# Kernel optimization log

Hardware: AMD Instinct MI355X
Metric: run time of the kernel (lower is better)

The kernel has to match this reference:

```python
import jax, jax.numpy as jnp
import numpy as np

N = 12288   # num_nodes
D = 128     # isize
K_TOP = 31  # k + 1, per top_k(similarities, self.k + 1)


def setup_inputs() -> dict:
    key = jax.random.key(0)
    features = jax.random.normal(key, (N, D), dtype=jnp.float32)
    eye = jnp.eye(D, dtype=jnp.float32)  # param_init: weight <- I, bias <- 0
    return {
        "features": features,
        "W1": eye,
        "b1": jnp.zeros((D,), jnp.float32),
        "W2": eye,
        "b2": jnp.zeros((D,), jnp.float32),
    }


def reference(features, W1, b1, W2, b2):
    # internal_forward: Linear -> ReLU -> Linear (nlayers=2, act='relu')
    h = jax.nn.relu(features @ W1.T + b1)
    h = h @ W2.T + b2
    # F.normalize(h, dim=1, p=2) with eps=1e-12
    hn = h / jnp.maximum(jnp.linalg.norm(h, axis=1, keepdims=True), 1e-12)
    # dense N x N cosine similarity
    sim = hn @ hn.T
    # top_k: keep top (k+1) entries per row, zero elsewhere; then apply_non_linearity='relu'
    vals, idx = jax.lax.top_k(sim, K_TOP)          # [N, K_TOP]
    rows = jnp.arange(sim.shape[0])[:, None]       # [N, 1]
    # relu(sim * mask) == scatter relu(top-k values) into a zero matrix
    out = jnp.zeros_like(sim).at[rows, idx].set(jax.nn.relu(vals))
    return out
```

## Files before the change

kernel.cpp:

```cpp
#include <hip/hip_runtime.h>
#include <stdint.h>
#include <math.h>

#define NN 12288
#define DD 128
#define KTOP 31
#define TCAND 64
#define CCAP 128
#define RPB 16
#define WPB 8
#define LDEP 14
#define NSTREAM 32
#define KPR (NSTREAM * LDEP)
#define KPL (KPR / 64)
#define ITERS 48

typedef __attribute__((ext_vector_type(8))) short bf16x8;
typedef __attribute__((ext_vector_type(4))) float f32x4;

__device__ __forceinline__ unsigned short f2bf(float x) {
  unsigned int u = __float_as_uint(x);
  u += 0x7fffu + ((u >> 16) & 1u);
  return (unsigned short)(u >> 16);
}

__device__ __forceinline__ unsigned umed3(unsigned a, unsigned b, unsigned c) {
  unsigned d;
  asm("v_med3_u32 %0, %1, %2, %3" : "=v"(d) : "v"(a), "v"(b), "v"(c));
  return d;
}

#define PINS(P) { \
  const unsigned p_ = (P); \
  _Pragma("unroll") \
  for (int i_ = 0; i_ < LDEP - 1; ++i_) \
    L[i_] = umed3(p_, L[i_], L[i_ + 1]); \
  L[LDEP - 1] = L[LDEP - 1] > p_ ? L[LDEP - 1] : p_; }

__global__ __launch_bounds__(128)
void wtrans_kernel(const float* __restrict__ W1, const float* __restrict__ W2,
                   float* __restrict__ W1T, float* __restrict__ W2T) {
  const int r = blockIdx.x, c = threadIdx.x;
  W1T[(size_t)c * DD + r] = W1[(size_t)r * DD + c];
  W2T[(size_t)c * DD + r] = W2[(size_t)r * DD + c];
}

__global__ __launch_bounds__(256)
void mlp_norm_kernel(const float* __restrict__ feat,
                     const float* __restrict__ W1T, const float* __restrict__ b1,
                     const float* __restrict__ W2T, const float* __restrict__ b2,
                     double* __restrict__ hn64, unsigned short* __restrict__ hnb) {
  __shared__ double bufA[16][DD];
  __shared__ double bufB[16][DD];
  __shared__ double mnorm[16];
  const int t = threadIdx.x;
  const int c = t & 127;
  const int g = t >> 7;
  const int row0 = blockIdx.x * 16 + g * 8;

  #pragma unroll
  for (int rr = 0; rr < 8; ++rr)
    bufA[g * 8 + rr][c] = (double)feat[(size_t)(row0 + rr) * DD + c];
  __syncthreads();

  {
    double acc[8] = {0,0,0,0,0,0,0,0};
    for (int k = 0; k < DD; k += 2) {
      double w0 = (double)W1T[(size_t)k * DD + c];
      double w1 = (double)W1T[(size_t)(k + 1) * DD + c];
      #pragma unroll
      for (int rr = 0; rr < 8; ++rr) {
        double2 a2 = *(const double2*)(&bufA[g * 8 + rr][k]);
        acc[rr] = fma(w0, a2.x, acc[rr]);
        acc[rr] = fma(w1, a2.y, acc[rr]);
      }
    }
    double bb = (double)b1[c];
    #pragma unroll
    for (int rr = 0; rr < 8; ++rr)
      bufB[g * 8 + rr][c] = fmax(acc[rr] + bb, 0.0);
  }
  __syncthreads();
  {
    double acc[8] = {0,0,0,0,0,0,0,0};
    for (int k = 0; k < DD; k += 2) {
      double w0 = (double)W2T[(size_t)k * DD + c];
      double w1 = (double)W2T[(size_t)(k + 1) * DD + c];
      #pragma unroll
      for (int rr = 0; rr < 8; ++rr) {
        double2 a2 = *(const double2*)(&bufB[g * 8 + rr][k]);
        acc[rr] = fma(w0, a2.x, acc[rr]);
        acc[rr] = fma(w1, a2.y, acc[rr]);
      }
    }
    double bb = (double)b2[c];
    #pragma unroll
    for (int rr = 0; rr < 8; ++rr)
      bufA[g * 8 + rr][c] = acc[rr] + bb;
  }
  __syncthreads();

  const int lane = t & 63;
  const int w = t >> 6;
  #pragma unroll
  for (int r2 = 0; r2 < 4; ++r2) {
    int rr = w * 4 + r2;
    double x0 = bufA[rr][lane];
    double x1 = bufA[rr][lane + 64];
    double s = x0 * x0 + x1 * x1;
    #pragma unroll
    for (int d = 1; d < 64; d <<= 1)
      s += __shfl_xor(s, d);
    if (lane == 0) mnorm[rr] = fmax(sqrt(s), 1e-12);
  }
  __syncthreads();
  #pragma unroll
  for (int rr = 0; rr < 8; ++rr) {
    double v = bufA[g * 8 + rr][c] / mnorm[g * 8 + rr];
    hn64[(size_t)(row0 + rr) * DD + c] = v;
    hnb[(size_t)(row0 + rr) * DD + c] = f2bf((float)v);
  }
}

__global__ __launch_bounds__(512, 6)
void simsel_kernel(const unsigned short* __restrict__ hnb,
                   const double* __restrict__ hn64,
                   float* __restrict__ resval, int* __restrict__ rescol) {
  __shared__ unsigned keybuf[RPB][KPR + 1];
  __shared__ unsigned scand[WPB][CCAP];
  __shared__ double cres[WPB][CCAP];
  const int t = threadIdx.x, lane = t & 63, wv = t >> 6;
  const int m = lane & 15, quad = lane >> 4;
  const int row0 = blockIdx.x * RPB;

  bf16x8 afrag[4];
  #pragma unroll
  for (int kc = 0; kc < 4; ++kc)
    afrag[kc] = *(const bf16x8*)(hnb + (size_t)(row0 + m) * DD + kc * 32 + quad * 8);

  unsigned L[LDEP];
  #pragma unroll
  for (int i = 0; i < LDEP; ++i) L[i] = 0;

  for (int it = 0; it < ITERS; ++it) {
    const int cb = it * (WPB * 32) + wv * 32;
    f32x4 acc0 = {0.0f, 0.0f, 0.0f, 0.0f};
    f32x4 acc1 = {0.0f, 0.0f, 0.0f, 0.0f};
    #pragma unroll
    for (int kc = 0; kc < 4; ++kc) {
      bf16x8 b0 = *(const bf16x8*)(hnb + (size_t)(cb + m) * DD + kc * 32 + quad * 8);
      bf16x8 b1 = *(const bf16x8*)(hnb + (size_t)(cb + 16 + m) * DD + kc * 32 + quad * 8);
      acc0 = __builtin_amdgcn_mfma_f32_16x16x32_bf16(b0, afrag[kc], acc0, 0, 0, 0);
      acc1 = __builtin_amdgcn_mfma_f32_16x16x32_bf16(b1, afrag[kc], acc1, 0, 0, 0);
    }
    #pragma unroll
    for (int r = 0; r < 4; ++r) {
      {
        unsigned bf = f2bf(acc0[r]);
        unsigned s = (bf & 0x8000u) ? 0u : bf;
        unsigned p = (s << 16) | (unsigned)(cb + quad * 4 + r);
        PINS(p)
      }
      {
        unsigned bf = f2bf(acc1[r]);
        unsigned s = (bf & 0x8000u) ? 0u : bf;
        unsigned p = (s << 16) | (unsigned)(cb + 16 + quad * 4 + r);
        PINS(p)
      }
    }
  }

  #pragma unroll
  for (int d = 0; d < LDEP; ++d)
    keybuf[m][(wv * 4 + quad) * LDEP + d] = L[d];
  __syncthreads();

  for (int ii = 0; ii < 2; ++ii) {
    const int lr = wv * 2 + ii;
    const int grow = row0 + lr;
    unsigned k7[KPL];
    #pragma unroll
    for (int i = 0; i < KPL; ++i)
      k7[i] = keybuf[lr][lane * KPL + i];

    unsigned lo = 0, hi = 0xFFFFu;
    while (lo < hi) {
      unsigned mid = (lo + hi + 1) >> 1;
      int c = 0;
      #pragma unroll
      for (int i = 0; i < KPL; ++i) c += (int)((k7[i] >> 16) >= mid);
      #pragma unroll
      for (int d = 1; d < 64; d <<= 1) c += __shfl_xor(c, d);
      if (c >= TCAND) lo = mid; else hi = mid - 1;
    }
    const unsigned thr = lo;

    int cl = 0;
    #pragma unroll
    for (int i = 0; i < KPL; ++i) cl += (int)((k7[i] >> 16) >= thr);
    int pre = cl;
    #pragma unroll
    for (int d = 1; d < 64; d <<= 1) {
      int y = __shfl_up(pre, d);
      if (lane >= d) pre += y;
    }
    const int total = __shfl(pre, 63);
    const int nc = total < CCAP ? total : CCAP;
    int slot = pre - cl;
    #pragma unroll
    for (int i = 0; i < KPL; ++i) {
      if ((k7[i] >> 16) >= thr) {
        if (slot < CCAP) scand[wv][slot] = k7[i];
        ++slot;
      }
    }

    const double* arow = hn64 + (size_t)grow * DD;
    const int hl = lane >> 5;
    const int kl = (lane & 31) * 4;
    const double a0 = arow[kl], a1 = arow[kl + 1], a2 = arow[kl + 2], a3 = arow[kl + 3];
    const int ng = (nc + 1) >> 1;
    for (int g = 0; g < ng; ++g) {
      const int ci = 2 * g + hl;
      double partial = 0.0;
      if (ci < nc) {
        const int col = (int)(scand[wv][ci] & 0xFFFFu);
        const double* brow = hn64 + (size_t)col * DD + kl;
        double2 b01 = *(const double2*)(brow);
        double2 b23 = *(const double2*)(brow + 2);
        partial = fma(a0, b01.x, fma(a1, b01.y, fma(a2, b23.x, a3 * b23.y)));
      }
      #pragma unroll
      for (int d = 1; d < 32; d <<= 1)
        partial += __shfl_xor(partial, d);
      if ((lane & 31) == 0 && ci < nc) cres[wv][ci] = partial;
    }
    double rv0 = -1.0e300, rv1 = -1.0e300;
    int rc0 = 0x7fffffff, rc1 = 0x7fffffff;
    if (lane < nc)      { rv0 = cres[wv][lane];      rc0 = (int)(scand[wv][lane] & 0xFFFFu); }
    if (lane + 64 < nc) { rv1 = cres[wv][lane + 64]; rc1 = (int)(scand[wv][lane + 64] & 0xFFFFu); }

    for (int itk = 0; itk < KTOP; ++itk) {
      bool f = (rv0 > rv1) || (rv0 == rv1 && rc0 < rc1);
      double bv = f ? rv0 : rv1;
      int bc = f ? rc0 : rc1;
      #pragma unroll
      for (int d = 1; d < 64; d <<= 1) {
        double ov = __shfl_xor(bv, d);
        int    oc = __shfl_xor(bc, d);
        bool tk = (ov > bv) || (ov == bv && oc < bc);
        bv = tk ? ov : bv;
        bc = tk ? oc : bc;
      }
      if (lane == itk) {
        resval[(size_t)grow * KTOP + itk] = (float)fmax(bv, 0.0);
        rescol[(size_t)grow * KTOP + itk] = bc;
      }
      if (rv0 == bv && rc0 == bc) rv0 = -1.0e300;
      else if (rv1 == bv && rc1 == bc) rv1 = -1.0e300;
    }
  }
}

__global__ __launch_bounds__(256)
void emit_kernel(const float* __restrict__ resval, const int* __restrict__ rescol,
                 float* __restrict__ out) {
  const int row = blockIdx.x, t = threadIdx.x;
  float v = 0.0f; int c = 0;
  if (t < KTOP) {
    v = resval[(size_t)row * KTOP + t];
    c = rescol[(size_t)row * KTOP + t];
  }
  f32x4* orow = (f32x4*)(out + (size_t)row * NN);
  const f32x4 z = {0.0f, 0.0f, 0.0f, 0.0f};
  #pragma unroll
  for (int i = 0; i < NN / 4 / 256; ++i)
    __builtin_nontemporal_store(z, &orow[i * 256 + t]);
  __syncthreads();
  if (t < KTOP) out[(size_t)row * NN + c] = v;
}

extern "C" void kernel_launch(void* const* d_in, const int* in_sizes, int n_in,
                              void* d_out, int out_size, void* d_ws, size_t ws_size,
                              hipStream_t stream) {
  const float* feat = (const float*)d_in[0];
  const float* W1 = (const float*)d_in[1];
  const float* b1 = (const float*)d_in[2];
  const float* W2 = (const float*)d_in[3];
  const float* b2 = (const float*)d_in[4];
  float* out = (float*)d_out;

  double* hn64 = (double*)d_ws;
  unsigned short* hnb = (unsigned short*)(hn64 + (size_t)NN * DD);
  float* resval = (float*)(hnb + (size_t)NN * DD);
  int* rescol = (int*)(resval + (size_t)NN * KTOP);
  float* W1T = (float*)(rescol + (size_t)NN * KTOP);
  float* W2T = W1T + DD * DD;

  wtrans_kernel<<<DD, DD, 0, stream>>>(W1, W2, W1T, W2T);
  mlp_norm_kernel<<<NN / 16, 256, 0, stream>>>(feat, W1T, b1, W2T, b2, hn64, hnb);
  simsel_kernel<<<NN / RPB, 512, 0, stream>>>(hnb, hn64, resval, rescol);
  emit_kernel<<<NN, 256, 0, stream>>>(resval, rescol, out);
}
```

Before: 1.066 ms.

## Stage candidate tiles in LDS via async global_load_lds double buffering

```diff
diff --git a/kernel.cpp b/kernel.cpp
--- a/kernel.cpp
+++ b/kernel.cpp
@@ -13,7 +13,8 @@
 #define NSTREAM 32
 #define KPR (NSTREAM * LDEP)
 #define KPL (KPR / 64)
-#define ITERS 48
+#define SC 128
+#define NST (NN / SC)
 
 typedef __attribute__((ext_vector_type(8))) short bf16x8;
 typedef __attribute__((ext_vector_type(4))) float f32x4;
@@ -122,10 +123,11 @@
   }
 }
 
-__global__ __launch_bounds__(512, 6)
+__global__ __launch_bounds__(512, 2)
 void simsel_kernel(const unsigned short* __restrict__ hnb,
                    const double* __restrict__ hn64,
                    float* __restrict__ resval, int* __restrict__ rescol) {
+  __shared__ __attribute__((aligned(16))) unsigned short stage[2][SC * DD];
   __shared__ unsigned keybuf[RPB][KPR + 1];
   __shared__ unsigned scand[WPB][CCAP];
   __shared__ double cres[WPB][CCAP];
@@ -138,36 +140,59 @@
   for (int kc = 0; kc < 4; ++kc)
     afrag[kc] = *(const bf16x8*)(hnb + (size_t)(row0 + m) * DD + kc * 32 + quad * 8);
 
+  const unsigned short* gsrc[4];
+  unsigned ldsb[4];
+  #pragma unroll
+  for (int i = 0; i < 4; ++i) {
+    int u = i * 512 + t;
+    int col = u >> 4;
+    int ch = (u & 15) ^ (col & 7);
+    gsrc[i] = hnb + (size_t)col * DD + ch * 8;
+    ldsb[i] = (unsigned)(i * 8192 + wv * 1024);
+  }
+
+  unsigned roff[4];
+  #pragma unroll
+  for (int kc = 0; kc < 4; ++kc)
+    roff[kc] = (unsigned)((wv * 16 + m) * 256 + (((kc * 4 + quad) ^ (m & 7)) * 16));
+
   unsigned L[LDEP];
   #pragma unroll
   for (int i = 0; i < LDEP; ++i) L[i] = 0;
 
-  for (int it = 0; it < ITERS; ++it) {
-    const int cb = it * (WPB * 32) + wv * 32;
-    f32x4 acc0 = {0.0f, 0.0f, 0.0f, 0.0f};
-    f32x4 acc1 = {0.0f, 0.0f, 0.0f, 0.0f};
+  {
+    char* dst = (char*)stage[0];
+    #pragma unroll
+    for (int i = 0; i < 4; ++i)
+      __builtin_amdgcn_global_load_lds((const void*)gsrc[i], (void*)(dst + ldsb[i]), 16, 0, 0);
+  }
+  __syncthreads();
+
+  for (int s = 0; s < NST; ++s) {
+    if (s + 1 < NST) {
+      char* dst = (char*)stage[(s + 1) & 1];
+      const size_t gadd = (size_t)(s + 1) * (SC * DD);
+      #pragma unroll
+      for (int i = 0; i < 4; ++i)
+        __builtin_amdgcn_global_load_lds((const void*)(gsrc[i] + gadd),
+                                         (void*)(dst + ldsb[i]), 16, 0, 0);
+    }
+    const char* buf = (const char*)stage[s & 1];
+    f32x4 acc = {0.0f, 0.0f, 0.0f, 0.0f};
     #pragma unroll
     for (int kc = 0; kc < 4; ++kc) {
-      bf16x8 b0 = *(const bf16x8*)(hnb + (size_t)(cb + m) * DD + kc * 32 + quad * 8);
-      bf16x8 b1 = *(const bf16x8*)(hnb + (size_t)(cb + 16 + m) * DD + kc * 32 + quad * 8);
-      acc0 = __builtin_amdgcn_mfma_f32_16x16x32_bf16(b0, afrag[kc], acc0, 0, 0, 0);
-      acc1 = __builtin_amdgcn_mfma_f32_16x16x32_bf16(b1, afrag[kc], acc1, 0, 0, 0);
-    }
+      bf16x8 b = *(const bf16x8*)(buf + roff[kc]);
+      acc = __builtin_amdgcn_mfma_f32_16x16x32_bf16(b, afrag[kc], acc, 0, 0, 0);
+    }
+    const int cbw = s * SC + wv * 16;
     #pragma unroll
     for (int r = 0; r < 4; ++r) {
-      {
-        unsigned bf = f2bf(acc0[r]);
-        unsigned s = (bf & 0x8000u) ? 0u : bf;
-        unsigned p = (s << 16) | (unsigned)(cb + quad * 4 + r);
-        PINS(p)
-      }
-      {
-        unsigned bf = f2bf(acc1[r]);
-        unsigned s = (bf & 0x8000u) ? 0u : bf;
-        unsigned p = (s << 16) | (unsigned)(cb + 16 + quad * 4 + r);
-        PINS(p)
-      }
-    }
+      unsigned bf = f2bf(acc[r]);
+      unsigned sc = (bf & 0x8000u) ? 0u : bf;
+      unsigned p = (sc << 16) | (unsigned)(cbw + quad * 4 + r);
+      PINS(p)
+    }
+    __syncthreads();
   }
 
   #pragma unroll
```

Result: slower. 1.179 ms (+10.6%).

## Split similarity ladder and candidate selection into separate kernels

Applied to the files above, without the earlier changes.

```diff
diff --git a/kernel.cpp b/kernel.cpp
--- a/kernel.cpp
+++ b/kernel.cpp
@@ -9,10 +9,7 @@
 #define CCAP 128
 #define RPB 16
 #define WPB 8
-#define LDEP 14
-#define NSTREAM 32
-#define KPR (NSTREAM * LDEP)
-#define KPL (KPR / 64)
+#define LDEP 8
 #define ITERS 48
 
 typedef __attribute__((ext_vector_type(8))) short bf16x8;
@@ -30,12 +27,12 @@
   return d;
 }
 
-#define PINS(P) { \
+#define PINS8(Lx, P) { \
   const unsigned p_ = (P); \
   _Pragma("unroll") \
-  for (int i_ = 0; i_ < LDEP - 1; ++i_) \
-    L[i_] = umed3(p_, L[i_], L[i_ + 1]); \
-  L[LDEP - 1] = L[LDEP - 1] > p_ ? L[LDEP - 1] : p_; }
+  for (int i_ = 0; i_ < 7; ++i_) \
+    Lx[i_] = umed3(p_, Lx[i_], Lx[i_ + 1]); \
+  Lx[7] = Lx[7] > p_ ? Lx[7] : p_; }
 
 __global__ __launch_bounds__(128)
 void wtrans_kernel(const float* __restrict__ W1, const float* __restrict__ W2,
@@ -123,12 +120,8 @@
 }
 
 __global__ __launch_bounds__(512, 6)
-void simsel_kernel(const unsigned short* __restrict__ hnb,
-                   const double* __restrict__ hn64,
-                   float* __restrict__ resval, int* __restrict__ rescol) {
-  __shared__ unsigned keybuf[RPB][KPR + 1];
-  __shared__ unsigned scand[WPB][CCAP];
-  __shared__ double cres[WPB][CCAP];
+void simladder_kernel(const unsigned short* __restrict__ hnb,
+                      unsigned* __restrict__ kbuf) {
   const int t = threadIdx.x, lane = t & 63, wv = t >> 6;
   const int m = lane & 15, quad = lane >> 4;
   const int row0 = blockIdx.x * RPB;
@@ -138,9 +131,8 @@
   for (int kc = 0; kc < 4; ++kc)
     afrag[kc] = *(const bf16x8*)(hnb + (size_t)(row0 + m) * DD + kc * 32 + quad * 8);
 
-  unsigned L[LDEP];
-  #pragma unroll
-  for (int i = 0; i < LDEP; ++i) L[i] = 0;
+  unsigned LA[8] = {0,0,0,0,0,0,0,0};
+  unsigned LB[8] = {0,0,0,0,0,0,0,0};
 
   for (int it = 0; it < ITERS; ++it) {
     const int cb = it * (WPB * 32) + wv * 32;
@@ -159,106 +151,117 @@
         unsigned bf = f2bf(acc0[r]);
         unsigned s = (bf & 0x8000u) ? 0u : bf;
         unsigned p = (s << 16) | (unsigned)(cb + quad * 4 + r);
-        PINS(p)
+        PINS8(LA, p)
       }
       {
         unsigned bf = f2bf(acc1[r]);
         unsigned s = (bf & 0x8000u) ? 0u : bf;
         unsigned p = (s << 16) | (unsigned)(cb + 16 + quad * 4 + r);
-        PINS(p)
+        PINS8(LB, p)
       }
     }
   }
 
-  #pragma unroll
-  for (int d = 0; d < LDEP; ++d)
-    keybuf[m][(wv * 4 + quad) * LDEP + d] = L[d];
-  __syncthreads();
-
-  for (int ii = 0; ii < 2; ++ii) {
-    const int lr = wv * 2 + ii;
-    const int grow = row0 + lr;
-    unsigned k7[KPL];
-    #pragma unroll
-    for (int i = 0; i < KPL; ++i)
-      k7[i] = keybuf[lr][lane * KPL + i];
-
-    unsigned lo = 0, hi = 0xFFFFu;
-    while (lo < hi) {
-      unsigned mid = (lo + hi + 1) >> 1;
-      int c = 0;
-      #pragma unroll
-      for (int i = 0; i < KPL; ++i) c += (int)((k7[i] >> 16) >= mid);
-      #pragma unroll
-      for (int d = 1; d < 64; d <<= 1) c += __shfl_xor(c, d);
-      if (c >= TCAND) lo = mid; else hi = mid - 1;
-    }
-    const unsigned thr = lo;
-
-    int cl = 0;
-    #pragma unroll
-    for (int i = 0; i < KPL; ++i) cl += (int)((k7[i] >> 16) >= thr);
-    int pre = cl;
+  unsigned* dst = kbuf + (size_t)(row0 + m) * 512 + (wv * 4 + quad) * 16;
+  *(uint4*)(dst)      = make_uint4(LA[0], LA[1], LA[2], LA[3]);
+  *(uint4*)(dst + 4)  = make_uint4(LA[4], LA[5], LA[6], LA[7]);
+  *(uint4*)(dst + 8)  = make_uint4(LB[0], LB[1], LB[2], LB[3]);
+  *(uint4*)(dst + 12) = make_uint4(LB[4], LB[5], LB[6], LB[7]);
+}
+
+__global__ __launch_bounds__(256)
+void select_kernel(const unsigned* __restrict__ kbuf,
+                   const double* __restrict__ hn64,
+                   float* __restrict__ resval, int* __restrict__ rescol) {
+  __shared__ unsigned scand[4][CCAP];
+  __shared__ double cres[4][CCAP];
+  const int t = threadIdx.x, lane = t & 63, wv = t >> 6;
+  const int row = blockIdx.x * 4 + wv;
+
+  unsigned k8[8];
+  {
+    const unsigned* src = kbuf + (size_t)row * 512 + lane * 8;
+    uint4 a = *(const uint4*)(src);
+    uint4 b = *(const uint4*)(src + 4);
+    k8[0] = a.x; k8[1] = a.y; k8[2] = a.z; k8[3] = a.w;
+    k8[4] = b.x; k8[5] = b.y; k8[6] = b.z; k8[7] = b.w;
+  }
+
+  unsigned lo = 0, hi = 0xFFFFu;
+  while (lo < hi) {
+    unsigned mid = (lo + hi + 1) >> 1;
+    int c = 0;
+    #pragma unroll
+    for (int i = 0; i < 8; ++i) c += (int)((k8[i] >> 16) >= mid);
+    #pragma unroll
+    for (int d = 1; d < 64; d <<= 1) c += __shfl_xor(c, d);
+    if (c >= TCAND) lo = mid; else hi = mid - 1;
+  }
+  const unsigned thr = lo;
+
+  int cl = 0;
+  #pragma unroll
+  for (int i = 0; i < 8; ++i) cl += (int)((k8[i] >> 16) >= thr);
+  int pre = cl;
+  #pragma unroll
+  for (int d = 1; d < 64; d <<= 1) {
+    int y = __shfl_up(pre, d);
+    if (lane >= d) pre += y;
+  }
+  const int total = __shfl(pre, 63);
+  const int nc = total < CCAP ? total : CCAP;
+  int slot = pre - cl;
+  #pragma unroll
+  for (int i = 0; i < 8; ++i) {
+    if ((k8[i] >> 16) >= thr) {
+      if (slot < CCAP) scand[wv][slot] = k8[i];
+      ++slot;
+    }
+  }
+
+  const double* arow = hn64 + (size_t)row * DD;
+  const int hl = lane >> 5;
+  const int kl = (lane & 31) * 4;
+  const double a0 = arow[kl], a1 = arow[kl + 1], a2 = arow[kl + 2], a3 = arow[kl + 3];
+  const int ng = (nc + 1) >> 1;
+  for (int g = 0; g < ng; ++g) {
+    const int ci = 2 * g + hl;
+    double partial = 0.0;
+    if (ci < nc) {
+      const int col = (int)(scand[wv][ci] & 0xFFFFu);
+      const double* brow = hn64 + (size_t)col * DD + kl;
+      double2 b01 = *(const double2*)(brow);
+      double2 b23 = *(const double2*)(brow + 2);
+      partial = fma(a0, b01.x, fma(a1, b01.y, fma(a2, b23.x, a3 * b23.y)));
+    }
+    #pragma unroll
+    for (int d = 1; d < 32; d <<= 1)
+      partial += __shfl_xor(partial, d);
+    if ((lane & 31) == 0 && ci < nc) cres[wv][ci] = partial;
+  }
+  double rv0 = -1.0e300, rv1 = -1.0e300;
+  int rc0 = 0x7fffffff, rc1 = 0x7fffffff;
+  if (lane < nc)      { rv0 = cres[wv][lane];      rc0 = (int)(scand[wv][lane] & 0xFFFFu); }
+  if (lane + 64 < nc) { rv1 = cres[wv][lane + 64]; rc1 = (int)(scand[wv][lane + 64] & 0xFFFFu); }
+
+  for (int itk = 0; itk < KTOP; ++itk) {
+    bool f = (rv0 > rv1) || (rv0 == rv1 && rc0 < rc1);
+    double bv = f ? rv0 : rv1;
+    int bc = f ? rc0 : rc1;
     #pragma unroll
     for (int d = 1; d < 64; d <<= 1) {
-      int y = __shfl_up(pre, d);
-      if (lane >= d) pre += y;
-    }
-    const int total = __shfl(pre, 63);
-    const int nc = total < CCAP ? total : CCAP;
-    int slot = pre - cl;
-    #pragma unroll
-    for (int i = 0; i < KPL; ++i) {
-      if ((k7[i] >> 16) >= thr) {
-        if (slot < CCAP) scand[wv][slot] = k7[i];
-        ++slot;
-      }
-    }
-
-    const double* arow = hn64 + (size_t)grow * DD;
-    const int hl = lane >> 5;
-    const int kl = (lane & 31) * 4;
-    const double a0 = arow[kl], a1 = arow[kl + 1], a2 = arow[kl + 2], a3 = arow[kl + 3];
-    const int ng = (nc + 1) >> 1;
-    for (int g = 0; g < ng; ++g) {
-      const int ci = 2 * g + hl;
-      double partial = 0.0;
-      if (ci < nc) {
-        const int col = (int)(scand[wv][ci] & 0xFFFFu);
-        const double* brow = hn64 + (size_t)col * DD + kl;
-        double2 b01 = *(const double2*)(brow);
-        double2 b23 = *(const double2*)(brow + 2);
-        partial = fma(a0, b01.x, fma(a1, b01.y, fma(a2, b23.x, a3 * b23.y)));
-      }
-      #pragma unroll
-      for (int d = 1; d < 32; d <<= 1)
-        partial += __shfl_xor(partial, d);
-      if ((lane & 31) == 0 && ci < nc) cres[wv][ci] = partial;
-    }
-    double rv0 = -1.0e300, rv1 = -1.0e300;
-    int rc0 = 0x7fffffff, rc1 = 0x7fffffff;
-    if (lane < nc)      { rv0 = cres[wv][lane];      rc0 = (int)(scand[wv][lane] & 0xFFFFu); }
-    if (lane + 64 < nc) { rv1 = cres[wv][lane + 64]; rc1 = (int)(scand[wv][lane + 64] & 0xFFFFu); }
-
-    for (int itk = 0; itk < KTOP; ++itk) {
-      bool f = (rv0 > rv1) || (rv0 == rv1 && rc0 < rc1);
-      double bv = f ? rv0 : rv1;
-      int bc = f ? rc0 : rc1;
-      #pragma unroll
-      for (int d = 1; d < 64; d <<= 1) {
-        double ov = __shfl_xor(bv, d);
-        int    oc = __shfl_xor(bc, d);
-        bool tk = (ov > bv) || (ov == bv && oc < bc);
-        bv = tk ? ov : bv;
-        bc = tk ? oc : bc;
-      }
-      if (lane == itk) {
-        resval[(size_t)grow * KTOP + itk] = (float)fmax(bv, 0.0);
-        rescol[(size_t)grow * KTOP + itk] = bc;
-      }
-      if (rv0 == bv && rc0 == bc) rv0 = -1.0e300;
-      else if (rv1 == bv && rc1 == bc) rv1 = -1.0e300;
-    }
+      double ov = __shfl_xor(bv, d);
+      int    oc = __shfl_xor(bc, d);
+      bool tk = (ov > bv) || (ov == bv && oc < bc);
+      bv = tk ? ov : bv;
+      bc = tk ? oc : bc;
+    }
+    if (lane == itk) {
+      resval[(size_t)row * KTOP + itk] = (float)fmax(bv, 0.0);
+      rescol[(size_t)row * KTOP + itk] = bc;
+    }
+    if (rv0 == bv && rc0 == bc) rv0 = -1.0e300;
+    else if (rv1 == bv && rc1 == bc) rv1 = -1.0e300;
   }
 }
 
@@ -297,8 +300,11 @@
   float* W1T = (float*)(rescol + (size_t)NN * KTOP);
   float* W2T = W1T + DD * DD;
 
+  unsigned* kbuf = (unsigned*)((char*)d_out + ((size_t)512 << 20));
+
   wtrans_kernel<<<DD, DD, 0, stream>>>(W1, W2, W1T, W2T);
   mlp_norm_kernel<<<NN / 16, 256, 0, stream>>>(feat, W1T, b1, W2T, b2, hn64, hnb);
-  simsel_kernel<<<NN / RPB, 512, 0, stream>>>(hnb, hn64, resval, rescol);
+  simladder_kernel<<<NN / RPB, 512, 0, stream>>>(hnb, kbuf);
+  select_kernel<<<NN / 4, 256, 0, stream>>>(kbuf, hn64, resval, rescol);
   emit_kernel<<<NN, 256, 0, stream>>>(resval, rescol, out);
 }
```

Measured after the change: 1.093 ms. 1.03x slower.
